# Optimization experiments

Measured on AMD Instinct MI355X. Metric: run time of the kernel, lower is better.

The kernel has to match this reference:

```python
import jax, jax.numpy as jnp
import numpy as np


def _sq_cdist(a, b):
    # squared Euclidean distances, [N, M]
    a2 = jnp.sum(a * a, axis=1)[:, None]
    b2 = jnp.sum(b * b, axis=1)[None, :]
    d = a2 + b2 - 2.0 * (a @ b.T)
    return jnp.maximum(d, 0.0)


def _gaussian_kernel_mean(a, b, sigmas):
    # mean over N*M of sum_k exp(-dist / (2*sigma_k))
    dist = _sq_cdist(a, b)                      # [N, M]
    beta = 1.0 / (2.0 * sigmas)                 # [K]
    s = jnp.exp(-beta[:, None, None] * dist[None, :, :])  # [K, N, M]
    return jnp.mean(jnp.sum(s, axis=0))


def setup_inputs() -> dict:
    key = jax.random.key(0)
    k1, k2 = jax.random.split(key)
    B, C, H, W = 4, 256, 32, 32
    x = jax.random.normal(k1, (B, C, H, W), dtype=jnp.float32)
    y = jax.random.normal(k2, (B, C, H, W), dtype=jnp.float32)
    sigmas = jnp.array([0.01, 0.1, 1.0, 10.0, 100.0], dtype=jnp.float32)
    return {"x": x, "y": y, "sigmas": sigmas}


def reference(x, y, sigmas):
    B, C, H, W = x.shape
    # (B,C,H,W) -> (B*H*W, C), matching flatten(2).transpose(1,2).reshape(-1,C)
    xf = jnp.transpose(x.reshape(B, C, H * W), (0, 2, 1)).reshape(-1, C)
    yf = jnp.transpose(y.reshape(B, C, H * W), (0, 2, 1)).reshape(-1, C)
    xx = _gaussian_kernel_mean(xf, xf, sigmas)
    yy = _gaussian_kernel_mean(yf, yf, sigmas)
    xy = _gaussian_kernel_mean(xf, yf, sigmas)
    return xx + yy - 2.0 * xy
```

## Files before the change

### kernel.cpp

```cpp
#include <hip/hip_runtime.h>
#include <hip/hip_bf16.h>


#define NSIG 5
#define CKS   262144
#define NBLK2 2080

typedef __attribute__((ext_vector_type(8))) short short8;
typedef __attribute__((ext_vector_type(4))) float floatx4;

#define GLDS16(gp, lp) __builtin_amdgcn_global_load_lds( \
    (const __attribute__((address_space(1))) void*)(gp),  \
    (__attribute__((address_space(3))) void*)(lp), 16, 0, 0)

__global__ __launch_bounds__(256) void prep_kernel(const float* __restrict__ x,
                                                   const float* __restrict__ y,
                                                   ushort* __restrict__ Zc,
                                                   float* __restrict__ norms) {
    const int bid = blockIdx.x;
    const int t = threadIdx.x;
    const int s = bid >> 8;
    const int b = (bid >> 6) & 3;
    const int p0 = (bid & 63) << 4;
    const float* src = s ? y : x;
    const int n0 = (s << 12) + (b << 10) + p0;

    __shared__ float tile[256][17];

    const int cg = t >> 2;
    const int p4 = (t & 3) << 2;
#pragma unroll
    for (int pass = 0; pass < 4; ++pass) {
        const int c = cg + (pass << 6);
        const float4 v = *(const float4*)(src + (((size_t)((b << 8) + c)) << 10) + p0 + p4);
        tile[c][p4] = v.x; tile[c][p4 + 1] = v.y; tile[c][p4 + 2] = v.z; tile[c][p4 + 3] = v.w;
    }
    __syncthreads();

    const int r = t >> 4;
    const int q = t & 15;
    const int row = n0 + r;
    const int sw = (row >> 1) & 3;
    float nsum = 0.f;
#pragma unroll
    for (int h = 0; h < 2; ++h) {
        const int j = q + (h << 4);
        const int ck = j >> 2;
        const int sq = (j & 3) ^ sw;
        const int c0 = j << 3;
        uint pk[4];
#pragma unroll
        for (int jj = 0; jj < 4; ++jj) {
            const float f0 = tile[c0 + 2 * jj][r];
            const float f1 = tile[c0 + 2 * jj + 1][r];
            const __hip_bfloat16 h0 = __float2bfloat16(f0);
            const __hip_bfloat16 h1 = __float2bfloat16(f1);
            const float q0 = __bfloat162float(h0), q1 = __bfloat162float(h1);
            nsum = fmaf(q0, q0, nsum);
            nsum = fmaf(q1, q1, nsum);
            pk[jj] = (uint)(*(const ushort*)&h0) | ((uint)(*(const ushort*)&h1) << 16);
        }
        *(uint4*)(Zc + (size_t)ck * CKS + (size_t)row * 32 + (sq << 3)) =
            make_uint4(pk[0], pk[1], pk[2], pk[3]);
    }
#pragma unroll
    for (int off = 1; off < 16; off <<= 1) nsum += __shfl_xor(nsum, off, 32);
    if (q == 0) norms[row] = nsum;
}

__global__ __launch_bounds__(256, 2) void gemm_epi(const ushort* __restrict__ Zc,
                                                   const float* __restrict__ norms,
                                                   const float* __restrict__ sigmas,
                                                   float* __restrict__ partials) {
    __shared__ ushort bufA[2][4096];
    __shared__ ushort bufB[2][4096];
    __shared__ float wsum[4];

    const int t = threadIdx.x;
    const int w = t >> 6, l = t & 63;
    const int m = l & 15, q = l >> 4;

    const int lin = blockIdx.x;
    int p = (int)((-4.0f + sqrtf(16.0f + 128.0f * (float)lin)) * (1.0f / 64.0f));
    p = p < 0 ? 0 : (p > 7 ? 7 : p);
    while (p < 7 && 32 * (p + 1) * (p + 1) + 4 * (p + 1) <= lin) ++p;
    while (p > 0 && 32 * p * p + 4 * p > lin) --p;
    const int o = lin - (32 * p * p + 4 * p);
    int c = 7;
#pragma unroll
    for (int cc = 7; cc >= 1; --cc) {
        const int Q = cc * (8 * p + 1) + (cc * (cc - 1)) / 2;
        if (o < Q) c = cc - 1;
    }
    const int Qc = c * (8 * p + 1) + (c * (c - 1)) / 2;
    const int tj2 = 8 * p + c;
    const int ti2 = o - Qc;
    const bool diagST = (ti2 == tj2);

    const int I0 = ti2 << 7;
    const int J0 = tj2 << 7;

    const int ti = (ti2 << 1) + (w >> 1);
    const int tj = (tj2 << 1) + (w & 1);
    const bool active = (ti <= tj);
    const bool diag = (ti == tj);
    const int i0 = ti << 6, j0 = tj << 6;

    int loffA[4], loffB[4];
#pragma unroll
    for (int f = 0; f < 4; ++f) {
        const int ra = ((w >> 1) << 6) + (f << 4) + m;
        loffA[f] = (ra << 5) + ((q ^ ((ra >> 1) & 3)) << 3);
        const int rb = ((w & 1) << 6) + (f << 4) + m;
        loffB[f] = (rb << 5) + ((q ^ ((rb >> 1) & 3)) << 3);
    }

    const int sg = (w << 10) + (l << 3);
    const ushort* gA0 = Zc + (size_t)I0 * 32 + sg;
    const ushort* gB0 = Zc + (size_t)J0 * 32 + sg;
    ushort* lA = &bufA[0][w << 10];
    ushort* lB = &bufB[0][w << 10];

    GLDS16(gA0, lA);
    GLDS16(gA0 + 512, lA + 512);
    if (!diagST) {
        GLDS16(gB0, lB);
        GLDS16(gB0 + 512, lB + 512);
    }
    __syncthreads();

    floatx4 accf[4][4];
#pragma unroll
    for (int fi = 0; fi < 4; ++fi)
#pragma unroll
        for (int fj = 0; fj < 4; ++fj) accf[fi][fj] = (floatx4){0.f, 0.f, 0.f, 0.f};

#pragma unroll
    for (int ck = 0; ck < 8; ++ck) {
        const int half = ck & 1;
        if (ck < 7) {
            const size_t ko = (size_t)(ck + 1) * CKS;
            ushort* nA = &bufA[half ^ 1][w << 10];
            GLDS16(gA0 + ko, nA);
            GLDS16(gA0 + ko + 512, nA + 512);
            if (!diagST) {
                ushort* nB = &bufB[half ^ 1][w << 10];
                GLDS16(gB0 + ko, nB);
                GLDS16(gB0 + ko + 512, nB + 512);
            }
        }
        const ushort* rA = &bufA[half][0];
        const ushort* rB = diagST ? &bufA[half][0] : &bufB[half][0];
        short8 fa[4], fb[4];
#pragma unroll
        for (int f = 0; f < 4; ++f) fa[f] = *(const short8*)(rA + loffA[f]);
#pragma unroll
        for (int f = 0; f < 4; ++f) fb[f] = *(const short8*)(rB + loffB[f]);
#pragma unroll
        for (int fi = 0; fi < 4; ++fi)
#pragma unroll
            for (int fj = 0; fj < 4; ++fj)
                accf[fi][fj] = __builtin_amdgcn_mfma_f32_16x16x32_bf16(fa[fi], fb[fj], accf[fi][fj], 0, 0, 0);
        __syncthreads();
    }

    float lsum = 0.f;
    if (active) {
        float c2[NSIG];
#pragma unroll
        for (int k = 0; k < NSIG; ++k) c2[k] = (-0.5f / sigmas[k]) * 1.44269504f;

        const float sgn2 = ((i0 < 4096) == (j0 < 4096)) ? 2.f : -2.f;

        float njs[4];
#pragma unroll
        for (int fj = 0; fj < 4; ++fj) njs[fj] = norms[j0 + (fj << 4) + m];

#pragma unroll
        for (int fi = 0; fi < 4; ++fi) {
            const floatx4 ni4 = *(const floatx4*)(norms + i0 + (fi << 4) + (q << 2));
#pragma unroll
            for (int fj = 0; fj < 4; ++fj) {
#pragma unroll
                for (int v = 0; v < 4; ++v) {
                    float d = fmaf(-2.f, accf[fi][fj][v], ni4[v] + njs[fj]);
                    d = fmaxf(d, 0.f);
                    if (diag) {
                        const int dif = ((fi - fj) << 4) + ((q << 2) + v) - m;
                        d = (dif < 0) ? d : 3.0e9f;
                    }
                    accf[fi][fj][v] = d;
                }
            }
        }

        float dmin = accf[0][0][0];
#pragma unroll
        for (int fi = 0; fi < 4; ++fi)
#pragma unroll
            for (int fj = 0; fj < 4; ++fj)
#pragma unroll
                for (int v = 0; v < 4; ++v) dmin = fminf(dmin, accf[fi][fj][v]);
#pragma unroll
        for (int off = 1; off < 64; off <<= 1) dmin = fminf(dmin, __shfl_xor(dmin, off, 64));

        float tsum = 0.f;
#pragma unroll
        for (int k = 0; k < NSIG; ++k) {
            if (c2[k] * dmin >= -126.f) {
#pragma unroll
                for (int fi = 0; fi < 4; ++fi)
#pragma unroll
                    for (int fj = 0; fj < 4; ++fj)
#pragma unroll
                        for (int v = 0; v < 4; ++v)
                            tsum += __builtin_amdgcn_exp2f(c2[k] * accf[fi][fj][v]);
            }
        }
        lsum = sgn2 * tsum;
    }

#pragma unroll
    for (int off = 32; off > 0; off >>= 1) lsum += __shfl_down(lsum, off, 64);
    if (l == 0) wsum[w] = lsum;
    __syncthreads();
    if (t == 0) partials[blockIdx.x] = wsum[0] + wsum[1] + wsum[2] + wsum[3];
}

__global__ __launch_bounds__(256) void finalize_kernel(const float* __restrict__ partials,
                                                       float* __restrict__ out) {
    __shared__ double sh[256];
    const int t = threadIdx.x;
    double s = 0.0;
    for (int i = t; i < NBLK2; i += 256) s += (double)partials[i];
    sh[t] = s;
    __syncthreads();
    for (int st = 128; st > 0; st >>= 1) {
        if (t < st) sh[t] += sh[t + st];
        __syncthreads();
    }
    if (t == 0) out[0] = (float)((sh[0] + 8192.0 * NSIG) * (1.0 / (4096.0 * 4096.0)));
}

extern "C" void kernel_launch(void* const* d_in, const int* in_sizes, int n_in,
                              void* d_out, int out_size, void* d_ws, size_t ws_size,
                              hipStream_t stream) {
    const float* x   = (const float*)d_in[0];
    const float* y   = (const float*)d_in[1];
    const float* sig = (const float*)d_in[2];

    ushort* Zc      = (ushort*)d_ws;
    float* norms    = (float*)((char*)d_ws + (size_t)8192 * 256 * 2);
    float* partials = (float*)((char*)norms + 8192 * sizeof(float));
    float* out      = (float*)d_out;

    prep_kernel<<<512, 256, 0, stream>>>(x, y, Zc, norms);
    gemm_epi<<<NBLK2, 256, 0, stream>>>(Zc, norms, sig, partials);
    finalize_kernel<<<1, 256, 0, stream>>>(partials, out);
}
```

Baseline: 96.86 us.

## Triple-buffer LDS loads with vmcnt-based waits and prefetch distance two

Switches the GEMM K-loop from double to triple buffering in LDS, issuing global-to-LDS loads two chunks ahead. The full __syncthreads is replaced with explicit s_waitcnt vmcnt plus raw s_barrier, so the newest chunk's loads can stay in flight across the barrier. The diagonal-tile special case that skipped B loads is removed, and the occupancy hint of two blocks per SM is dropped. This adds more LDS per block and redundant loads on diagonal tiles.

```diff
diff --git a/kernel.cpp b/kernel.cpp
--- a/kernel.cpp
+++ b/kernel.cpp
@@ -12,6 +12,9 @@
 #define GLDS16(gp, lp) __builtin_amdgcn_global_load_lds( \
     (const __attribute__((address_space(1))) void*)(gp),  \
     (__attribute__((address_space(3))) void*)(lp), 16, 0, 0)
+
+#define WAITVM4 asm volatile("s_waitcnt vmcnt(4)" ::: "memory")
+#define WAITVM0 asm volatile("s_waitcnt vmcnt(0)" ::: "memory")
 
 __global__ __launch_bounds__(256) void prep_kernel(const float* __restrict__ x,
                                                    const float* __restrict__ y,
@@ -68,12 +71,12 @@
     if (q == 0) norms[row] = nsum;
 }
 
-__global__ __launch_bounds__(256, 2) void gemm_epi(const ushort* __restrict__ Zc,
-                                                   const float* __restrict__ norms,
-                                                   const float* __restrict__ sigmas,
-                                                   float* __restrict__ partials) {
-    __shared__ ushort bufA[2][4096];
-    __shared__ ushort bufB[2][4096];
+__global__ __launch_bounds__(256) void gemm_epi(const ushort* __restrict__ Zc,
+                                                const float* __restrict__ norms,
+                                                const float* __restrict__ sigmas,
+                                                float* __restrict__ partials) {
+    __shared__ ushort bufA[3][4096];
+    __shared__ ushort bufB[3][4096];
     __shared__ float wsum[4];
 
     const int t = threadIdx.x;
@@ -95,7 +98,6 @@
     const int Qc = c * (8 * p + 1) + (c * (c - 1)) / 2;
     const int tj2 = 8 * p + c;
     const int ti2 = o - Qc;
-    const bool diagST = (ti2 == tj2);
 
     const int I0 = ti2 << 7;
     const int J0 = tj2 << 7;
@@ -118,16 +120,19 @@
     const int sg = (w << 10) + (l << 3);
     const ushort* gA0 = Zc + (size_t)I0 * 32 + sg;
     const ushort* gB0 = Zc + (size_t)J0 * 32 + sg;
-    ushort* lA = &bufA[0][w << 10];
-    ushort* lB = &bufB[0][w << 10];
-
-    GLDS16(gA0, lA);
-    GLDS16(gA0 + 512, lA + 512);
-    if (!diagST) {
-        GLDS16(gB0, lB);
-        GLDS16(gB0 + 512, lB + 512);
-    }
-    __syncthreads();
+    const int lo = w << 10;
+
+    GLDS16(gA0,        &bufA[0][lo]);
+    GLDS16(gA0 + 512,  &bufA[0][lo + 512]);
+    GLDS16(gB0,        &bufB[0][lo]);
+    GLDS16(gB0 + 512,  &bufB[0][lo + 512]);
+    GLDS16(gA0 + CKS,       &bufA[1][lo]);
+    GLDS16(gA0 + CKS + 512, &bufA[1][lo + 512]);
+    GLDS16(gB0 + CKS,       &bufB[1][lo]);
+    GLDS16(gB0 + CKS + 512, &bufB[1][lo + 512]);
+    WAITVM4;
+    __builtin_amdgcn_s_barrier();
+    __builtin_amdgcn_sched_barrier(0);
 
     floatx4 accf[4][4];
 #pragma unroll
@@ -137,31 +142,31 @@
 
 #pragma unroll
     for (int ck = 0; ck < 8; ++ck) {
-        const int half = ck & 1;
-        if (ck < 7) {
-            const size_t ko = (size_t)(ck + 1) * CKS;
-            ushort* nA = &bufA[half ^ 1][w << 10];
-            GLDS16(gA0 + ko, nA);
-            GLDS16(gA0 + ko + 512, nA + 512);
-            if (!diagST) {
-                ushort* nB = &bufB[half ^ 1][w << 10];
-                GLDS16(gB0 + ko, nB);
-                GLDS16(gB0 + ko + 512, nB + 512);
-            }
-        }
-        const ushort* rA = &bufA[half][0];
-        const ushort* rB = diagST ? &bufA[half][0] : &bufB[half][0];
+        const ushort* rA = &bufA[ck % 3][0];
+        const ushort* rB = &bufB[ck % 3][0];
         short8 fa[4], fb[4];
 #pragma unroll
         for (int f = 0; f < 4; ++f) fa[f] = *(const short8*)(rA + loffA[f]);
 #pragma unroll
         for (int f = 0; f < 4; ++f) fb[f] = *(const short8*)(rB + loffB[f]);
+        if (ck < 6) {
+            const size_t ko = (size_t)(ck + 2) * CKS;
+            const int nb = (ck + 2) % 3;
+            GLDS16(gA0 + ko,       &bufA[nb][lo]);
+            GLDS16(gA0 + ko + 512, &bufA[nb][lo + 512]);
+            GLDS16(gB0 + ko,       &bufB[nb][lo]);
+            GLDS16(gB0 + ko + 512, &bufB[nb][lo + 512]);
+        }
 #pragma unroll
         for (int fi = 0; fi < 4; ++fi)
 #pragma unroll
             for (int fj = 0; fj < 4; ++fj)
                 accf[fi][fj] = __builtin_amdgcn_mfma_f32_16x16x32_bf16(fa[fi], fb[fj], accf[fi][fj], 0, 0, 0);
-        __syncthreads();
+        if (ck < 7) {
+            if (ck < 6) { WAITVM4; } else { WAITVM0; }
+            __builtin_amdgcn_s_barrier();
+            __builtin_amdgcn_sched_barrier(0);
+        }
     }
 
     float lsum = 0.f;
```

After: 95.70 us. Within noise of the previous version (-1.2%).

## Deepen GEMM LDS pipeline to four stages and remap block order for XCDs

Applied to the files above, without the earlier changes.

Replaces the double-buffered K-loop with a four-stage LDS ring. All four initial chunks are prefetched, and explicit vmcnt waits plus raw barriers throttle each chunk. Block IDs are remapped with a stride of 260 so that neighbouring tiles land on the same XCD. The diagonal-tile special case that skipped loading B is removed, so diagonal blocks now load B redundantly. LDS use doubles to 64KB per block, which may limit occupancy against the 2-blocks-per-CU launch bound.

```diff
diff --git a/kernel.cpp b/kernel.cpp
--- a/kernel.cpp
+++ b/kernel.cpp
@@ -72,15 +72,16 @@
                                                    const float* __restrict__ norms,
                                                    const float* __restrict__ sigmas,
                                                    float* __restrict__ partials) {
-    __shared__ ushort bufA[2][4096];
-    __shared__ ushort bufB[2][4096];
-    __shared__ float wsum[4];
+    __shared__ ushort bufA[4][4096];
+    __shared__ ushort bufB[4][4096];
 
     const int t = threadIdx.x;
     const int w = t >> 6, l = t & 63;
     const int m = l & 15, q = l >> 4;
 
-    const int lin = blockIdx.x;
+    const int bid = blockIdx.x;
+    const int lin = (bid & 7) * 260 + (bid >> 3);
+
     int p = (int)((-4.0f + sqrtf(16.0f + 128.0f * (float)lin)) * (1.0f / 64.0f));
     p = p < 0 ? 0 : (p > 7 ? 7 : p);
     while (p < 7 && 32 * (p + 1) * (p + 1) + 4 * (p + 1) <= lin) ++p;
@@ -95,7 +96,6 @@
     const int Qc = c * (8 * p + 1) + (c * (c - 1)) / 2;
     const int tj2 = 8 * p + c;
     const int ti2 = o - Qc;
-    const bool diagST = (ti2 == tj2);
 
     const int I0 = ti2 << 7;
     const int J0 = tj2 << 7;
@@ -118,16 +118,17 @@
     const int sg = (w << 10) + (l << 3);
     const ushort* gA0 = Zc + (size_t)I0 * 32 + sg;
     const ushort* gB0 = Zc + (size_t)J0 * 32 + sg;
-    ushort* lA = &bufA[0][w << 10];
-    ushort* lB = &bufB[0][w << 10];
-
-    GLDS16(gA0, lA);
-    GLDS16(gA0 + 512, lA + 512);
-    if (!diagST) {
-        GLDS16(gB0, lB);
-        GLDS16(gB0 + 512, lB + 512);
-    }
-    __syncthreads();
+    const int lo = w << 10;
+
+#define STAGE(k) do {                                                   \
+        const size_t ko_ = (size_t)(k) * CKS; const int s_ = (k) & 3;   \
+        GLDS16(gA0 + ko_,       &bufA[s_][lo]);                         \
+        GLDS16(gA0 + ko_ + 512, &bufA[s_][lo + 512]);                   \
+        GLDS16(gB0 + ko_,       &bufB[s_][lo]);                         \
+        GLDS16(gB0 + ko_ + 512, &bufB[s_][lo + 512]);                   \
+    } while (0)
+
+    STAGE(0); STAGE(1); STAGE(2); STAGE(3);
 
     floatx4 accf[4][4];
 #pragma unroll
@@ -135,34 +136,33 @@
 #pragma unroll
         for (int fj = 0; fj < 4; ++fj) accf[fi][fj] = (floatx4){0.f, 0.f, 0.f, 0.f};
 
-#pragma unroll
-    for (int ck = 0; ck < 8; ++ck) {
-        const int half = ck & 1;
-        if (ck < 7) {
-            const size_t ko = (size_t)(ck + 1) * CKS;
-            ushort* nA = &bufA[half ^ 1][w << 10];
-            GLDS16(gA0 + ko, nA);
-            GLDS16(gA0 + ko + 512, nA + 512);
-            if (!diagST) {
-                ushort* nB = &bufB[half ^ 1][w << 10];
-                GLDS16(gB0 + ko, nB);
-                GLDS16(gB0 + ko + 512, nB + 512);
-            }
-        }
-        const ushort* rA = &bufA[half][0];
-        const ushort* rB = diagST ? &bufA[half][0] : &bufB[half][0];
-        short8 fa[4], fb[4];
-#pragma unroll
-        for (int f = 0; f < 4; ++f) fa[f] = *(const short8*)(rA + loffA[f]);
-#pragma unroll
-        for (int f = 0; f < 4; ++f) fb[f] = *(const short8*)(rB + loffB[f]);
-#pragma unroll
-        for (int fi = 0; fi < 4; ++fi)
-#pragma unroll
-            for (int fj = 0; fj < 4; ++fj)
-                accf[fi][fj] = __builtin_amdgcn_mfma_f32_16x16x32_bf16(fa[fi], fb[fj], accf[fi][fj], 0, 0, 0);
-        __syncthreads();
-    }
+#define CHUNK(k, N) do {                                                 \
+        asm volatile("s_waitcnt vmcnt(" #N ")" ::: "memory");            \
+        __builtin_amdgcn_s_barrier();                                    \
+        __builtin_amdgcn_sched_barrier(0);                               \
+        const ushort* rA_ = &bufA[(k) & 3][0];                           \
+        const ushort* rB_ = &bufB[(k) & 3][0];                           \
+        short8 fa_[4], fb_[4];                                           \
+        _Pragma("unroll")                                                \
+        for (int f = 0; f < 4; ++f) fa_[f] = *(const short8*)(rA_ + loffA[f]); \
+        _Pragma("unroll")                                                \
+        for (int f = 0; f < 4; ++f) fb_[f] = *(const short8*)(rB_ + loffB[f]); \
+        _Pragma("unroll")                                                \
+        for (int fi = 0; fi < 4; ++fi)                                   \
+            _Pragma("unroll")                                            \
+            for (int fj = 0; fj < 4; ++fj)                               \
+                accf[fi][fj] = __builtin_amdgcn_mfma_f32_16x16x32_bf16(  \
+                    fa_[fi], fb_[fj], accf[fi][fj], 0, 0, 0);            \
+        __builtin_amdgcn_s_barrier();                                    \
+        __builtin_amdgcn_sched_barrier(0);                               \
+        if ((k) + 4 < 8) STAGE((k) + 4);                                 \
+    } while (0)
+
+    CHUNK(0, 12); CHUNK(1, 12); CHUNK(2, 12); CHUNK(3, 12);
+    CHUNK(4, 12); CHUNK(5, 8);  CHUNK(6, 4);  CHUNK(7, 0);
+
+#undef CHUNK
+#undef STAGE
 
     float lsum = 0.f;
     if (active) {
@@ -222,9 +222,11 @@
 
 #pragma unroll
     for (int off = 32; off > 0; off >>= 1) lsum += __shfl_down(lsum, off, 64);
+    __syncthreads();
+    float* wsum = (float*)&bufA[0][0];
     if (l == 0) wsum[w] = lsum;
     __syncthreads();
-    if (t == 0) partials[blockIdx.x] = wsum[0] + wsum[1] + wsum[2] + wsum[3];
+    if (t == 0) partials[bid] = wsum[0] + wsum[1] + wsum[2] + wsum[3];
 }
 
 __global__ __launch_bounds__(256) void finalize_kernel(const float* __restrict__ partials,
```

Result: slower. 104.9 us (+8.3%).
